# Optimization experiments

Measured on AMD Instinct MI355X. Metric: run time of the kernel, lower is better.

## Reference

```python
import jax, jax.numpy as jnp
import numpy as np

# dims
B, L, C = 2, 2048, 256          # batch, seq_len (== max_length), input_dim
H, D = 8, 32                     # num_head, head_dim
W = 3                            # avg-pool window along key axis


def setup_inputs() -> dict:
    key = jax.random.key(0)
    ks = jax.random.split(key, 7)
    g_qk = (2.0 / (C + H * D)) ** 0.5   # GlorotNormal std
    g_v = (2.0 / (C + H)) ** 0.5
    g_pe = (2.0 / (L + C)) ** 0.5
    return {
        "x":  jax.random.normal(ks[0], (B, L, C), dtype=jnp.float32),
        "Wq": jax.random.normal(ks[1], (C, H * D), dtype=jnp.float32) * g_qk,
        "bq": jnp.zeros((H, 1, 1, D), dtype=jnp.float32),
        "Wk": jax.random.normal(ks[2], (C, H * D), dtype=jnp.float32) * g_qk,
        "bk": jnp.zeros((H, 1, 1, D), dtype=jnp.float32),
        "Wv": jax.random.normal(ks[3], (C, H), dtype=jnp.float32) * g_v,
        "pe": jax.random.normal(ks[4], (L, C), dtype=jnp.float32) * g_pe,
    }


def reference(x, Wq, bq, Wk, bk, Wv, pe):
    b, l, _ = x.shape
    xq = x + pe                                   # (B,L,C) -- pe added to q and k inputs only
    q = (xq @ Wq).reshape(b, l, H, D).transpose(2, 0, 1, 3) + bq   # (H,B,L,D)
    k = (xq @ Wk).reshape(b, l, H, D).transpose(2, 0, 1, 3) + bk   # (H,B,L,D)
    v = (x @ Wv).transpose(2, 0, 1)               # (H,B,L) scalar gate per (head, pos)

    attn = jnp.einsum('hbqd,hbkd->hbqk', q, k) * (float(D) ** -0.5)  # (H,B,Lq,Lk)
    attn = jax.nn.softmax(attn, axis=-1)
    # band_part(-1, 0): keep lower triangle (q >= k), applied AFTER softmax
    causal = jnp.tril(jnp.ones((l, l), dtype=bool))
    attn = jnp.where(causal, attn, jnp.zeros((), attn.dtype))
    # scalar value gate along the query axis
    attn = attn * v[..., None]                    # (H,B,Lq,Lk)
    # avg-pool window W along key axis, SAME padding, pads excluded from count (TF semantics)
    sums = jax.lax.reduce_window(attn, 0.0, jax.lax.add, (1, 1, 1, W), (1, 1, 1, 1), 'SAME')
    counts = jax.lax.reduce_window(jnp.ones((l,), attn.dtype), 0.0, jax.lax.add, (W,), (1,), 'SAME')
    attn = sums / counts                          # broadcast (Lk,) over (H,B,Lq,Lk)
    # permute to (B,Lq,Lk,H) then global_mode sum over Lq  ->  (B,Lk,H)
    return jnp.sum(attn, axis=2).transpose(1, 2, 0)
```

## Files before the change

kernel.cpp:

```cpp
#include <hip/hip_runtime.h>

#define B 2
#define L 2048
#define C 256
#define H 8
#define D 32
#define HB 16
#define SCALE 0.17677669529663687f
#define LOG2E 1.4426950408889634f

using bf16x8 = __attribute__((ext_vector_type(8))) __bf16;
using f32x4  = __attribute__((ext_vector_type(4))) float;

static __device__ inline unsigned short f2bf(float f) {
    unsigned u = __float_as_uint(f);
    return (unsigned short)((u + 0x7fffu + ((u >> 16) & 1u)) >> 16);
}

static __device__ inline float fexp2(float x) {
#if __has_builtin(__builtin_amdgcn_exp2f)
    return __builtin_amdgcn_exp2f(x);
#else
    float r; asm("v_exp_f32 %0, %1" : "=v"(r) : "v"(x)); return r;
#endif
}

__global__ __launch_bounds__(256) void proj_kernel(
    const float* __restrict__ x,
    const float* __restrict__ Wq,
    const float* __restrict__ bq,
    const float* __restrict__ Wk,
    const float* __restrict__ bk,
    const float* __restrict__ Wv,
    const float* __restrict__ pe,
    unsigned short* __restrict__ Qo,
    unsigned short* __restrict__ Ko,
    float* __restrict__ Vo)
{
    __shared__ float xqT[C][8];
    __shared__ float xrT[C][8];
    __shared__ float vred[4][8][8];
    const int t = threadIdx.x;
    const int row0 = blockIdx.x * 8;
    const int b = row0 >> 11;

#pragma unroll
    for (int i = 0; i < 8; ++i) {
        const int row = row0 + i;
        const int l = row & (L - 1);
        const float xv = x[row * C + t];
        xrT[t][i] = xv;
        xqT[t][i] = xv + pe[l * C + t];
    }
    __syncthreads();

    float accq[8], acck[8];
#pragma unroll
    for (int i = 0; i < 8; ++i) { accq[i] = 0.f; acck[i] = 0.f; }

#pragma unroll 4
    for (int c = 0; c < C; ++c) {
        const float wq = Wq[c * (H * D) + t];
        const float wk = Wk[c * (H * D) + t];
        const float4 xa = *(const float4*)&xqT[c][0];
        const float4 xb = *(const float4*)&xqT[c][4];
        accq[0] += xa.x * wq; acck[0] += xa.x * wk;
        accq[1] += xa.y * wq; acck[1] += xa.y * wk;
        accq[2] += xa.z * wq; acck[2] += xa.z * wk;
        accq[3] += xa.w * wq; acck[3] += xa.w * wk;
        accq[4] += xb.x * wq; acck[4] += xb.x * wk;
        accq[5] += xb.y * wq; acck[5] += xb.y * wk;
        accq[6] += xb.z * wq; acck[6] += xb.z * wk;
        accq[7] += xb.w * wq; acck[7] += xb.w * wk;
    }

    const int h = t >> 5, d = t & 31;
    const float bqv = bq[t];
    const float bkv = bk[t];
#pragma unroll
    for (int i = 0; i < 8; ++i) {
        const int l = (row0 + i) & (L - 1);
        const size_t o = ((size_t)(h * B + b) * L + l) * D + d;
        Qo[o] = f2bf((accq[i] + bqv) * (SCALE * LOG2E));
        Ko[o] = f2bf(acck[i] + bkv);
    }

    {
        const int cc = t >> 6, sub = t & 63, vi = sub >> 3, vh = sub & 7;
        float va = 0.f;
        for (int c = cc * 64; c < cc * 64 + 64; ++c)
            va += xrT[c][vi] * Wv[c * H + vh];
        vred[cc][vi][vh] = va;
    }
    __syncthreads();
    if (t < 64) {
        const int i2 = t >> 3, h2 = t & 7;
        const float v = vred[0][i2][h2] + vred[1][i2][h2] +
                        vred[2][i2][h2] + vred[3][i2][h2];
        const int l = (row0 + i2) & (L - 1);
        Vo[(h2 * B + b) * L + l] = v;
    }
}

__global__ __launch_bounds__(256) void passA_kernel(
    const __bf16* __restrict__ Qb, const __bf16* __restrict__ Kb,
    const float* __restrict__ V, float* __restrict__ G)
{
    __shared__ float lredA[4][4][4][16];
    __shared__ float lredB[4][4][4][16];
    const int tid = threadIdx.x;
    const int w = tid >> 6, lane = tid & 63;
    const int quad = lane >> 4, col = lane & 15;
    const int xcd = blockIdx.x & 7, g = blockIdx.x >> 3;
    const int hb = xcd * 2 + (g >> 6), p = g & 63;
    const __bf16* Qp = Qb + (size_t)hb * L * D;
    const __bf16* Kp = Kb + (size_t)hb * L * D;

    const bf16x8 qfa = *(const bf16x8*)(Qp + ((2 * p) * 16 + col) * D + quad * 8);
    const bf16x8 qfb = *(const bf16x8*)(Qp + ((2 * p + 1) * 16 + col) * D + quad * 8);
    const f32x4 zero = {0.f, 0.f, 0.f, 0.f};

    float la0 = 0.f, la1 = 0.f, la2 = 0.f, la3 = 0.f;
    float lb0 = 0.f, lb1 = 0.f, lb2 = 0.f, lb3 = 0.f;
    const __bf16* kp = Kp + (w * 512 + col) * D + quad * 8;
#pragma unroll 4
    for (int kt = 0; kt < 32; ++kt) {
        const bf16x8 kf = *(const bf16x8*)kp;
        kp += 16 * D;
        f32x4 a = __builtin_amdgcn_mfma_f32_16x16x32_bf16(qfa, kf, zero, 0, 0, 0);
        f32x4 bb = __builtin_amdgcn_mfma_f32_16x16x32_bf16(qfb, kf, zero, 0, 0, 0);
        la0 += fexp2(a[0]);  lb0 += fexp2(bb[0]);
        la1 += fexp2(a[1]);  lb1 += fexp2(bb[1]);
        la2 += fexp2(a[2]);  lb2 += fexp2(bb[2]);
        la3 += fexp2(a[3]);  lb3 += fexp2(bb[3]);
    }
    lredA[w][quad][0][col] = la0;  lredB[w][quad][0][col] = lb0;
    lredA[w][quad][1][col] = la1;  lredB[w][quad][1][col] = lb1;
    lredA[w][quad][2][col] = la2;  lredB[w][quad][2][col] = lb2;
    lredA[w][quad][3][col] = la3;  lredB[w][quad][3][col] = lb3;
    __syncthreads();
    if (tid < 32) {
        const int r8 = tid & 15;
        const int qd = r8 >> 2, r = r8 & 3;
        const float* base = (tid < 16) ? &lredA[0][0][0][0] : &lredB[0][0][0][0];
        float s = 0.f;
#pragma unroll
        for (int w2 = 0; w2 < 4; ++w2) {
            const float* pp = base + ((w2 * 4 + qd) * 4 + r) * 16;
#pragma unroll
            for (int c2 = 0; c2 < 16; ++c2) s += pp[c2];
        }
        const int qt = 2 * p + (tid >> 4);
        const int qq = hb * L + qt * 16 + r8;
        G[qq] = V[qq] / s;
    }
}

__global__ __launch_bounds__(256) void passB_kernel(
    const __bf16* __restrict__ Qb, const __bf16* __restrict__ Kb,
    const float* __restrict__ G, float* __restrict__ S)
{
    __shared__ float sred[2][4][4][16];
    const int tid = threadIdx.x;
    const int w = tid >> 6, lane = tid & 63;
    const int quad = lane >> 4, col = lane & 15;
    const int xcd = blockIdx.x & 7, g = blockIdx.x >> 3;
    const int hb = xcd * 2 + (g >> 6), p = g & 63;
    const int kb0 = 2 * p, kb1 = 2 * p + 1;
    const __bf16* Qp = Qb + (size_t)hb * L * D;
    const __bf16* Kp = Kb + (size_t)hb * L * D;
    const float* Gp = G + hb * L;

    const bf16x8 kf0 = *(const bf16x8*)(Kp + (kb0 * 16 + col) * D + quad * 8);
    const bf16x8 kf1 = *(const bf16x8*)(Kp + (kb1 * 16 + col) * D + quad * 8);
    const f32x4 zero = {0.f, 0.f, 0.f, 0.f};
    const int kidx0 = kb0 * 16 + col;
    const int kidx1 = kb1 * 16 + col;

    float s0 = 0.f, s1 = 0.f;
    int qt = kb0 + w;
    if (qt < 128) {
        const bf16x8 qf = *(const bf16x8*)(Qp + (qt * 16 + col) * D + quad * 8);
        const float4 gg = *(const float4*)(Gp + qt * 16 + quad * 4);
        const int qbase = qt * 16 + quad * 4;
        f32x4 a0 = __builtin_amdgcn_mfma_f32_16x16x32_bf16(qf, kf0, zero, 0, 0, 0);
        if (w == 0) {
            s0 += (qbase + 0 >= kidx0) ? fexp2(a0[0]) * gg.x : 0.f;
            s0 += (qbase + 1 >= kidx0) ? fexp2(a0[1]) * gg.y : 0.f;
            s0 += (qbase + 2 >= kidx0) ? fexp2(a0[2]) * gg.z : 0.f;
            s0 += (qbase + 3 >= kidx0) ? fexp2(a0[3]) * gg.w : 0.f;
        } else {
            s0 += fexp2(a0[0]) * gg.x + fexp2(a0[1]) * gg.y +
                  fexp2(a0[2]) * gg.z + fexp2(a0[3]) * gg.w;
            f32x4 a1 = __builtin_amdgcn_mfma_f32_16x16x32_bf16(qf, kf1, zero, 0, 0, 0);
            if (w == 1) {
                s1 += (qbase + 0 >= kidx1) ? fexp2(a1[0]) * gg.x : 0.f;
                s1 += (qbase + 1 >= kidx1) ? fexp2(a1[1]) * gg.y : 0.f;
                s1 += (qbase + 2 >= kidx1) ? fexp2(a1[2]) * gg.z : 0.f;
                s1 += (qbase + 3 >= kidx1) ? fexp2(a1[3]) * gg.w : 0.f;
            } else {
                s1 += fexp2(a1[0]) * gg.x + fexp2(a1[1]) * gg.y +
                      fexp2(a1[2]) * gg.z + fexp2(a1[3]) * gg.w;
            }
        }
        qt += 4;
    }
    for (; qt < 128; qt += 4) {
        const bf16x8 qf = *(const bf16x8*)(Qp + (qt * 16 + col) * D + quad * 8);
        const float4 gg = *(const float4*)(Gp + qt * 16 + quad * 4);
        f32x4 a0 = __builtin_amdgcn_mfma_f32_16x16x32_bf16(qf, kf0, zero, 0, 0, 0);
        f32x4 a1 = __builtin_amdgcn_mfma_f32_16x16x32_bf16(qf, kf1, zero, 0, 0, 0);
        s0 += fexp2(a0[0]) * gg.x + fexp2(a0[1]) * gg.y +
              fexp2(a0[2]) * gg.z + fexp2(a0[3]) * gg.w;
        s1 += fexp2(a1[0]) * gg.x + fexp2(a1[1]) * gg.y +
              fexp2(a1[2]) * gg.z + fexp2(a1[3]) * gg.w;
    }
    sred[0][w][quad][col] = s0;
    sred[1][w][quad][col] = s1;
    __syncthreads();
    if (tid < 32) {
        const int c = tid & 15, which = tid >> 4;
        float s = 0.f;
#pragma unroll
        for (int j = 0; j < 16; ++j) s += sred[which][j >> 2][j & 3][c];
        S[hb * L + (2 * p + which) * 16 + c] = s;
    }
}

__global__ __launch_bounds__(256) void pool_kernel(
    const float* __restrict__ S, float* __restrict__ out)
{
    const int flat = blockIdx.x * 256 + threadIdx.x;
    const int h = flat & 7;
    const int k = (flat >> 3) & (L - 1);
    const int b = flat >> 14;
    const float* Sb = S + (h * B + b) * L;
    float s = Sb[k];
    float cnt = 1.f;
    if (k > 0)     { s += Sb[k - 1]; cnt += 1.f; }
    if (k < L - 1) { s += Sb[k + 1]; cnt += 1.f; }
    out[flat] = s / cnt;
}

extern "C" void kernel_launch(void* const* d_in, const int* in_sizes, int n_in,
                              void* d_out, int out_size, void* d_ws, size_t ws_size,
                              hipStream_t stream)
{
    const float* x  = (const float*)d_in[0];
    const float* Wq = (const float*)d_in[1];
    const float* bq = (const float*)d_in[2];
    const float* Wk = (const float*)d_in[3];
    const float* bk = (const float*)d_in[4];
    const float* Wv = (const float*)d_in[5];
    const float* pe = (const float*)d_in[6];
    float* out = (float*)d_out;

    unsigned short* Qbf = (unsigned short*)d_ws;
    unsigned short* Kbf = Qbf + (size_t)HB * L * D;
    float* Vo = (float*)(Kbf + (size_t)HB * L * D);
    float* G  = Vo + (size_t)HB * L;
    float* S  = G  + (size_t)HB * L;

    proj_kernel<<<B * L / 8, 256, 0, stream>>>(x, Wq, bq, Wk, bk, Wv, pe,
                                               Qbf, Kbf, Vo);
    passA_kernel<<<1024, 256, 0, stream>>>(
        (const __bf16*)Qbf, (const __bf16*)Kbf, Vo, G);
    passB_kernel<<<1024, 256, 0, stream>>>(
        (const __bf16*)Qbf, (const __bf16*)Kbf, G, S);
    pool_kernel<<<(B * L * H) / 256, 256, 0, stream>>>(S, out);
}
```

Before: 118.1 us.

## Move Q/K projection to bf16 MFMA GEMM with pre-transposed weights

Replaces the scalar fp32 FMA projection kernel with two kernels. A prep kernel computes the V gate and transposes Wq/Wk into bf16, folding the softmax scale into Wq. A second kernel does the Q/K projection with 16x16x32 bf16 MFMA, using a swizzled LDS tile of x+pe. This cuts the FMA-bound projection cost but adds a kernel launch and rounds x+pe and the weights to bf16 before the matmul, which loses some precision.

```diff
diff --git a/kernel.cpp b/kernel.cpp
--- a/kernel.cpp
+++ b/kernel.cpp
@@ -8,6 +8,7 @@
 #define HB 16
 #define SCALE 0.17677669529663687f
 #define LOG2E 1.4426950408889634f
+#define QS (SCALE * LOG2E)
 
 using bf16x8 = __attribute__((ext_vector_type(8))) __bf16;
 using f32x4  = __attribute__((ext_vector_type(4))) float;
@@ -15,6 +16,9 @@
 static __device__ inline unsigned short f2bf(float f) {
     unsigned u = __float_as_uint(f);
     return (unsigned short)((u + 0x7fffu + ((u >> 16) & 1u)) >> 16);
+}
+static __device__ inline unsigned pk2(float lo, float hi) {
+    return (unsigned)f2bf(lo) | ((unsigned)f2bf(hi) << 16);
 }
 
 static __device__ inline float fexp2(float x) {
@@ -25,80 +29,137 @@
 #endif
 }
 
-__global__ __launch_bounds__(256) void proj_kernel(
+__global__ __launch_bounds__(256) void prep_kernel(
     const float* __restrict__ x,
     const float* __restrict__ Wq,
-    const float* __restrict__ bq,
     const float* __restrict__ Wk,
-    const float* __restrict__ bk,
     const float* __restrict__ Wv,
-    const float* __restrict__ pe,
-    unsigned short* __restrict__ Qo,
-    unsigned short* __restrict__ Ko,
+    unsigned short* __restrict__ WqT,
+    unsigned short* __restrict__ WkT,
     float* __restrict__ Vo)
 {
-    __shared__ float xqT[C][8];
-    __shared__ float xrT[C][8];
-    __shared__ float vred[4][8][8];
+    __shared__ float smem[64 * 65];
     const int t = threadIdx.x;
-    const int row0 = blockIdx.x * 8;
-    const int b = row0 >> 11;
-
-#pragma unroll
-    for (int i = 0; i < 8; ++i) {
-        const int row = row0 + i;
-        const int l = row & (L - 1);
-        const float xv = x[row * C + t];
-        xrT[t][i] = xv;
-        xqT[t][i] = xv + pe[l * C + t];
+
+    if (blockIdx.x < 512) {
+        float (*xrT)[8] = (float(*)[8])smem;
+        float* vred = smem + 256 * 8;
+        const int row0 = blockIdx.x * 8;
+        const int b = row0 >> 11;
+#pragma unroll
+        for (int i = 0; i < 8; ++i)
+            xrT[t][i] = x[(row0 + i) * C + t];
+        __syncthreads();
+        {
+            const int cc = t >> 6, sub = t & 63, vi = sub >> 3, vh = sub & 7;
+            float va = 0.f;
+            for (int c = cc * 64; c < cc * 64 + 64; ++c)
+                va += xrT[c][vi] * Wv[c * H + vh];
+            vred[(cc * 8 + vi) * 8 + vh] = va;
+        }
+        __syncthreads();
+        if (t < 64) {
+            const int i2 = t >> 3, h2 = t & 7;
+            const float v = vred[(0 * 8 + i2) * 8 + h2] + vred[(1 * 8 + i2) * 8 + h2] +
+                            vred[(2 * 8 + i2) * 8 + h2] + vred[(3 * 8 + i2) * 8 + h2];
+            const int l = (row0 + i2) & (L - 1);
+            Vo[(h2 * B + b) * L + l] = v;
+        }
+    } else {
+        const int bb = blockIdx.x - 512;
+        const int mat = bb >> 4;
+        const int tile = bb & 15, ci = tile >> 2, ni = tile & 3;
+        const float* W = mat ? Wk : Wq;
+        unsigned short* WT = mat ? WkT : WqT;
+        const float s = mat ? 1.0f : QS;
+        const int c0 = ci * 64, n0 = ni * 64;
+        float (*ld)[65] = (float(*)[65])smem;
+        const int tr = t >> 4, tc = (t & 15) * 4;
+#pragma unroll
+        for (int p = 0; p < 4; ++p) {
+            const int lc = p * 16 + tr;
+            const float4 v = *(const float4*)&W[(c0 + lc) * (H * D) + n0 + tc];
+            ld[lc][tc] = v.x; ld[lc][tc + 1] = v.y;
+            ld[lc][tc + 2] = v.z; ld[lc][tc + 3] = v.w;
+        }
+        __syncthreads();
+#pragma unroll
+        for (int p = 0; p < 4; ++p) {
+            const int nl = p * 16 + tr;
+            const unsigned lo = pk2(ld[tc][nl] * s, ld[tc + 1][nl] * s);
+            const unsigned hi = pk2(ld[tc + 2][nl] * s, ld[tc + 3][nl] * s);
+            uint2 u; u.x = lo; u.y = hi;
+            *(uint2*)&WT[(n0 + nl) * C + c0 + tc] = u;
+        }
+    }
+}
+
+__global__ __launch_bounds__(256) void qk_gemm_kernel(
+    const float* __restrict__ x, const float* __restrict__ pe,
+    const unsigned short* __restrict__ WqT, const unsigned short* __restrict__ WkT,
+    const float* __restrict__ bq, const float* __restrict__ bk,
+    unsigned short* __restrict__ Qo, unsigned short* __restrict__ Ko)
+{
+    __shared__ uint4 xqs[16][32];
+    const int t = threadIdx.x;
+    const int w = t >> 6, lane = t & 63;
+    const int quad = lane >> 4, col = lane & 15;
+    const int row0 = (blockIdx.x >> 2) * 16;
+    const int n0 = (blockIdx.x & 3) * 64;
+
+    {
+        const int srow = t >> 4, sc = (t & 15) * 16;
+        const int grow = row0 + srow;
+        const int gl = grow & (L - 1);
+        const float* xp = x + (size_t)grow * C + sc;
+        const float* pp = pe + (size_t)gl * C + sc;
+        const float4 a0 = ((const float4*)xp)[0], a1 = ((const float4*)xp)[1];
+        const float4 a2 = ((const float4*)xp)[2], a3 = ((const float4*)xp)[3];
+        const float4 p0 = ((const float4*)pp)[0], p1 = ((const float4*)pp)[1];
+        const float4 p2 = ((const float4*)pp)[2], p3 = ((const float4*)pp)[3];
+        uint4 u0, u1;
+        u0.x = pk2(a0.x + p0.x, a0.y + p0.y);
+        u0.y = pk2(a0.z + p0.z, a0.w + p0.w);
+        u0.z = pk2(a1.x + p1.x, a1.y + p1.y);
+        u0.w = pk2(a1.z + p1.z, a1.w + p1.w);
+        u1.x = pk2(a2.x + p2.x, a2.y + p2.y);
+        u1.y = pk2(a2.z + p2.z, a2.w + p2.w);
+        u1.z = pk2(a3.x + p3.x, a3.y + p3.y);
+        u1.w = pk2(a3.z + p3.z, a3.w + p3.w);
+        const int cb = (t & 15) * 2;
+        xqs[srow][(cb + 0) ^ (srow & 7)] = u0;
+        xqs[srow][(cb + 1) ^ (srow & 7)] = u1;
     }
     __syncthreads();
 
-    float accq[8], acck[8];
-#pragma unroll
-    for (int i = 0; i < 8; ++i) { accq[i] = 0.f; acck[i] = 0.f; }
-
-#pragma unroll 4
-    for (int c = 0; c < C; ++c) {
-        const float wq = Wq[c * (H * D) + t];
-        const float wk = Wk[c * (H * D) + t];
-        const float4 xa = *(const float4*)&xqT[c][0];
-        const float4 xb = *(const float4*)&xqT[c][4];
-        accq[0] += xa.x * wq; acck[0] += xa.x * wk;
-        accq[1] += xa.y * wq; acck[1] += xa.y * wk;
-        accq[2] += xa.z * wq; acck[2] += xa.z * wk;
-        accq[3] += xa.w * wq; acck[3] += xa.w * wk;
-        accq[4] += xb.x * wq; acck[4] += xb.x * wk;
-        accq[5] += xb.y * wq; acck[5] += xb.y * wk;
-        accq[6] += xb.z * wq; acck[6] += xb.z * wk;
-        accq[7] += xb.w * wq; acck[7] += xb.w * wk;
-    }
-
-    const int h = t >> 5, d = t & 31;
-    const float bqv = bq[t];
-    const float bkv = bk[t];
-#pragma unroll
-    for (int i = 0; i < 8; ++i) {
-        const int l = (row0 + i) & (L - 1);
+    bf16x8 af[8];
+#pragma unroll
+    for (int kk = 0; kk < 8; ++kk)
+        af[kk] = *(const bf16x8*)&xqs[col][(kk * 4 + quad) ^ (col & 7)];
+
+    const int n = n0 + w * 16 + col;
+    const unsigned short* wq = WqT + (size_t)n * C;
+    const unsigned short* wk = WkT + (size_t)n * C;
+    f32x4 accq = {0.f, 0.f, 0.f, 0.f};
+    f32x4 acck = {0.f, 0.f, 0.f, 0.f};
+#pragma unroll
+    for (int kk = 0; kk < 8; ++kk) {
+        const bf16x8 bq8 = *(const bf16x8*)(wq + kk * 32 + quad * 8);
+        const bf16x8 bk8 = *(const bf16x8*)(wk + kk * 32 + quad * 8);
+        accq = __builtin_amdgcn_mfma_f32_16x16x32_bf16(af[kk], bq8, accq, 0, 0, 0);
+        acck = __builtin_amdgcn_mfma_f32_16x16x32_bf16(af[kk], bk8, acck, 0, 0, 0);
+    }
+
+    const int h = n >> 5, d = n & 31;
+    const float bqv = bq[n] * QS;
+    const float bkv = bk[n];
+#pragma unroll
+    for (int r = 0; r < 4; ++r) {
+        const int m = quad * 4 + r;
+        const int grow = row0 + m, b = grow >> 11, l = grow & (L - 1);
         const size_t o = ((size_t)(h * B + b) * L + l) * D + d;
-        Qo[o] = f2bf((accq[i] + bqv) * (SCALE * LOG2E));
-        Ko[o] = f2bf(acck[i] + bkv);
-    }
-
-    {
-        const int cc = t >> 6, sub = t & 63, vi = sub >> 3, vh = sub & 7;
-        float va = 0.f;
-        for (int c = cc * 64; c < cc * 64 + 64; ++c)
-            va += xrT[c][vi] * Wv[c * H + vh];
-        vred[cc][vi][vh] = va;
-    }
-    __syncthreads();
-    if (t < 64) {
-        const int i2 = t >> 3, h2 = t & 7;
-        const float v = vred[0][i2][h2] + vred[1][i2][h2] +
-                        vred[2][i2][h2] + vred[3][i2][h2];
-        const int l = (row0 + i2) & (L - 1);
-        Vo[(h2 * B + b) * L + l] = v;
+        Qo[o] = f2bf(accq[r] + bqv);
+        Ko[o] = f2bf(acck[r] + bkv);
     }
 }
 
@@ -260,9 +321,11 @@
     float* Vo = (float*)(Kbf + (size_t)HB * L * D);
     float* G  = Vo + (size_t)HB * L;
     float* S  = G  + (size_t)HB * L;
-
-    proj_kernel<<<B * L / 8, 256, 0, stream>>>(x, Wq, bq, Wk, bk, Wv, pe,
-                                               Qbf, Kbf, Vo);
+    unsigned short* WqT = (unsigned short*)(S + (size_t)HB * L);
+    unsigned short* WkT = WqT + (size_t)C * H * D;
+
+    prep_kernel<<<544, 256, 0, stream>>>(x, Wq, Wk, Wv, WqT, WkT, Vo);
+    qk_gemm_kernel<<<1024, 256, 0, stream>>>(x, pe, WqT, WkT, bq, bk, Qbf, Kbf);
     passA_kernel<<<1024, 256, 0, stream>>>(
         (const __bf16*)Qbf, (const __bf16*)Kbf, Vo, G);
     passB_kernel<<<1024, 256, 0, stream>>>(
```

Measured after the change: 107.2 us. -9.3%, faster.
